# Kernel optimization log

Measured on AMD Instinct MI355X. Metric: run time of the kernel, lower is better.

## Reference

```python
import jax, jax.numpy as jnp
import numpy as np
import math

DIM = 192
D_CONV = 3
EXPAND = 2
D_INNER = EXPAND * DIM          # 384
D_STATE = 1                     # hard-coded in MambaLayer: StructureAwareSSM(..., d_state=1, ...)
DT_RANK = math.ceil(DIM / 16)   # 12
B_, H_, W_ = 16, 96, 96
EPS = 1e-5


def setup_inputs() -> dict:
    key = jax.random.key(0)
    ks = jax.random.split(key, 12)
    s = 0.02
    return {
        "x": jax.random.normal(ks[0], (B_, H_, W_, DIM), jnp.float32),
        "ln_w": jnp.ones((DIM,), jnp.float32),
        "ln_b": jnp.zeros((DIM,), jnp.float32),
        "W_in": jax.random.normal(ks[1], (DIM, 2 * D_INNER), jnp.float32) * s,
        "conv_w": jax.random.normal(ks[2], (D_INNER, 1, D_CONV), jnp.float32) * s,
        "conv_b": jnp.zeros((D_INNER,), jnp.float32),
        "W_xproj": jax.random.normal(ks[3], (D_INNER, DT_RANK + 2 * D_STATE), jnp.float32) * s,
        "W_dt": jax.random.normal(ks[4], (DT_RANK, D_INNER), jnp.float32) * s,
        "b_dt": jax.random.normal(ks[5], (D_INNER,), jnp.float32) * s,
        "A_log": jnp.log(jax.random.uniform(ks[6], (D_INNER, D_STATE), jnp.float32, 0.5, 1.5)),
        "D": jnp.ones((D_INNER,), jnp.float32),
        "W_out": jax.random.normal(ks[7], (D_INNER, DIM), jnp.float32) * s,
    }


def _layernorm(x, w, b):
    mu = x.mean(-1, keepdims=True)
    var = jnp.mean(jnp.square(x - mu), axis=-1, keepdims=True)
    return (x - mu) * jax.lax.rsqrt(var + EPS) * w + b


def _mamba(xs, W_in, conv_w, conv_b, W_xproj, W_dt, b_dt, A_log, D, W_out):
    # xs: (B, L, C)
    b, L, c = xs.shape
    xz = xs @ W_in                                  # (B,L,2*di)
    xb, z = jnp.split(xz, 2, axis=-1)
    # causal depthwise conv over sequence dim
    xc = jax.lax.conv_general_dilated(
        xb.transpose(0, 2, 1),                      # (B,di,L)
        conv_w,                                     # (di,1,k)
        window_strides=(1,),
        padding=[(D_CONV - 1, 0)],
        dimension_numbers=("NCH", "OIH", "NCH"),
        feature_group_count=D_INNER,
    ) + conv_b[None, :, None]
    u = jax.nn.silu(xc).transpose(0, 2, 1)          # (B,L,di)
    proj = u @ W_xproj                              # (B,L,dt_rank+2*ds)
    dt_r = proj[..., :DT_RANK]
    B_ssm = proj[..., DT_RANK:DT_RANK + D_STATE]    # (B,L,ds)
    C_ssm = proj[..., DT_RANK + D_STATE:]           # (B,L,ds)
    dt = jax.nn.softplus(dt_r @ W_dt + b_dt)        # (B,L,di)
    A = -jnp.exp(A_log)                             # (di,ds)
    dA = jnp.exp(dt[..., None] * A)                             # (B,L,di,ds)
    dBu = dt[..., None] * B_ssm[:, :, None, :] * u[..., None]   # (B,L,di,ds)

    def step(h, inp):
        dA_t, dBu_t = inp
        h = dA_t * h + dBu_t
        return h, h

    h0 = jnp.zeros((b, D_INNER, D_STATE), xs.dtype)
    _, hs = jax.lax.scan(step, h0, (dA.transpose(1, 0, 2, 3), dBu.transpose(1, 0, 2, 3)))
    # hs: (L,B,di,ds); contract over state with C
    y = jnp.einsum("lbis,bls->bli", hs, C_ssm)      # (B,L,di)
    y = y + u * D
    y = y * jax.nn.silu(z)
    return y @ W_out                                # (B,L,C)


def reference(x, ln_w, ln_b, W_in, conv_w, conv_b, W_xproj, W_dt, b_dt, A_log, D, W_out):
    b, h, w, c = x.shape
    xn = _layernorm(x, ln_w, ln_b)
    xs = xn.reshape(b, h * w, c)
    y = _mamba(xs, W_in, conv_w, conv_b, W_xproj, W_dt, b_dt, A_log, D, W_out)
    return y.reshape(b, h, w, c) + x
```

## Files before the change

kernel.cpp:

```cpp
#include <hip/hip_runtime.h>
#include <math.h>

#define DIMC 192
#define DIN 384
#define XZC 768
#define NPROJ 14
#define PSTR 16
#define LSEQ 9216
#define NBATCH 16
#define NTOK (NBATCH*LSEQ)
#define CHUNK 128
#define NCH (LSEQ/CHUNK)

typedef unsigned short u16;
typedef unsigned int u32;
typedef __attribute__((ext_vector_type(8))) short bf16x8;
typedef __attribute__((ext_vector_type(4))) float f32x4;

__device__ __forceinline__ float bf2f(u16 a){
  union { u32 u; float f; } v; v.u = ((u32)a)<<16; return v.f;
}
__device__ __forceinline__ u16 f2bf(float f){
  union { u32 u; float f; } v; v.f = f;
  u32 r = v.u + 0x7FFFu + ((v.u>>16)&1u);
  return (u16)(r>>16);
}
__device__ __forceinline__ float frcp(float x){ return __builtin_amdgcn_rcpf(x); }
__device__ __forceinline__ float softplus_f(float x){
  return fmaxf(x, 0.f) + __logf(1.f + __expf(-fabsf(x)));
}
__device__ __forceinline__ float silu_f(float a){
  return a * frcp(1.f + __expf(-a));
}

__global__ void k_convert(const float* __restrict__ Win, const float* __restrict__ Wout,
                          const float* __restrict__ Wx, const float* __restrict__ cw,
                          u16* __restrict__ Bp1, u16* __restrict__ Bp2,
                          u16* __restrict__ Wxp, float* __restrict__ cwT){
  int i = blockIdx.x*256 + threadIdx.x;
  if (i < XZC*DIMC){
    int j = i&7, lane = (i>>3)&63, rest = i>>9;
    int ks = rest%6, nt = rest/6;
    int k = ks*32 + (lane>>4)*8 + j, n = nt*16 + (lane&15);
    Bp1[i] = f2bf(Win[(size_t)k*XZC + n]);
  }
  if (i < DIN*DIMC){
    int j = i&7, lane = (i>>3)&63, rest = i>>9;
    int ks = rest%12, nt = rest/12;
    int k = ks*32 + (lane>>4)*8 + j, n = nt*16 + (lane&15);
    Bp2[i] = f2bf(Wout[(size_t)k*DIMC + n]);
  }
  if (i < 12*4*16*8){
    int j = i&7, n = (i>>3)&15, quad = (i>>7)&3, kstep = i>>9;
    int k = kstep*32 + quad*8 + j;
    Wxp[i] = (n < NPROJ) ? f2bf(Wx[k*NPROJ + n]) : (u16)0;
  }
  if (i < 3*DIN){
    int tap = i / DIN, ch = i - tap*DIN;
    cwT[i] = cw[ch*3 + tap];
  }
}

__global__ __launch_bounds__(256) void k_lngemm1(const float* __restrict__ x,
        const float* __restrict__ lnw, const float* __restrict__ lnb,
        const u16* __restrict__ Bp1, u16* __restrict__ xB, u16* __restrict__ zB)
{
  int tid = threadIdx.x, wv = tid>>6, lane = tid&63;
  int lr = lane&15, lq = lane>>4;
  int tokw = blockIdx.x*128 + wv*32;
  bf16x8 af[2][6];
  #pragma unroll
  for (int s=0;s<2;++s){
    int token = tokw + s*16 + lr;
    const float* xp = x + (size_t)token*DIMC + lq*8;
    float v[48];
    #pragma unroll
    for (int ks=0;ks<6;++ks){
      float4 a = *(const float4*)(xp + ks*32);
      float4 b = *(const float4*)(xp + ks*32 + 4);
      v[ks*8+0]=a.x; v[ks*8+1]=a.y; v[ks*8+2]=a.z; v[ks*8+3]=a.w;
      v[ks*8+4]=b.x; v[ks*8+5]=b.y; v[ks*8+6]=b.z; v[ks*8+7]=b.w;
    }
    float sm = 0.f;
    #pragma unroll
    for (int j=0;j<48;++j) sm += v[j];
    sm += __shfl_xor(sm, 16); sm += __shfl_xor(sm, 32);
    float mu = sm * (1.0f/DIMC);
    float q = 0.f;
    #pragma unroll
    for (int j=0;j<48;++j){ float d = v[j]-mu; q += d*d; }
    q += __shfl_xor(q, 16); q += __shfl_xor(q, 32);
    float rstd = rsqrtf(q*(1.0f/DIMC) + 1e-5f);
    #pragma unroll
    for (int ks=0;ks<6;++ks){
      const float* wp = lnw + lq*8 + ks*32;
      const float* bp = lnb + lq*8 + ks*32;
      float4 w0 = *(const float4*)(wp),   w1 = *(const float4*)(wp+4);
      float4 b0 = *(const float4*)(bp),   b1 = *(const float4*)(bp+4);
      float wj[8] = {w0.x,w0.y,w0.z,w0.w,w1.x,w1.y,w1.z,w1.w};
      float bj[8] = {b0.x,b0.y,b0.z,b0.w,b1.x,b1.y,b1.z,b1.w};
      #pragma unroll
      for (int j=0;j<8;++j)
        af[s][ks][j] = (short)f2bf((v[ks*8+j]-mu)*rstd*wj[j] + bj[j]);
    }
  }
  #pragma unroll 2
  for (int nt=0; nt<48; ++nt){
    f32x4 acc0 = (f32x4){0.f,0.f,0.f,0.f};
    f32x4 acc1 = (f32x4){0.f,0.f,0.f,0.f};
    #pragma unroll
    for (int ks=0;ks<6;++ks){
      bf16x8 bf_ = *(const bf16x8*)(Bp1 + (size_t)((nt*6+ks)<<9) + (size_t)lane*8);
      acc0 = __builtin_amdgcn_mfma_f32_16x16x32_bf16(af[0][ks], bf_, acc0, 0,0,0);
      acc1 = __builtin_amdgcn_mfma_f32_16x16x32_bf16(af[1][ks], bf_, acc1, 0,0,0);
    }
    int col = nt*16 + lr;
    u16* base = (col < DIN) ? xB : zB;
    int cc = (col < DIN) ? col : col - DIN;
    #pragma unroll
    for (int r=0;r<4;++r){
      int row0 = tokw + lq*4 + r;
      base[(size_t)row0*DIN + cc]      = f2bf(acc0[r]);
      base[(size_t)(row0+16)*DIN + cc] = f2bf(acc1[r]);
    }
  }
}

__global__ __launch_bounds__(256) void k_conv(const u16* __restrict__ xB,
        const float* __restrict__ cwT, const float* __restrict__ cb,
        const u16* __restrict__ Wxp, float* __restrict__ proj){
  int tid = threadIdx.x, wv = tid>>6, lane = tid&63;
  int lr = lane&15, lq = lane>>4;
  int tok0 = blockIdx.x*64 + wv*16;
  int token = tok0 + lr;
  int l = token % LSEQ;
  float m1 = (l>=1)?1.f:0.f, m2 = (l>=2)?1.f:0.f;
  int tm1 = (l>=1)? token-1 : token;
  int tm2 = (l>=2)? token-2 : token;
  bf16x8 bfrag[12];
  #pragma unroll
  for (int ks=0;ks<12;++ks)
    bfrag[ks] = *(const bf16x8*)(Wxp + (size_t)ks*512 + (size_t)lane*8);
  f32x4 acc = (f32x4){0.f,0.f,0.f,0.f};
  #pragma unroll
  for (int ks=0;ks<12;++ks){
    int ch0 = ks*32 + lq*8;
    bf16x8 x0 = *(const bf16x8*)(xB + (size_t)token*DIN + ch0);
    bf16x8 x1 = *(const bf16x8*)(xB + (size_t)tm1*DIN + ch0);
    bf16x8 x2 = *(const bf16x8*)(xB + (size_t)tm2*DIN + ch0);
    const float* w2 = cwT + 2*DIN + ch0;
    const float* w1 = cwT + 1*DIN + ch0;
    const float* w0 = cwT + 0*DIN + ch0;
    const float* cbp = cb + ch0;
    bf16x8 af;
    #pragma unroll
    for (int j=0;j<8;++j){
      float a = cbp[j] + w2[j]*bf2f((u16)x0[j])
                       + (w1[j]*m1)*bf2f((u16)x1[j])
                       + (w0[j]*m2)*bf2f((u16)x2[j]);
      af[j] = (short)f2bf(silu_f(a));
    }
    acc = __builtin_amdgcn_mfma_f32_16x16x32_bf16(af, bfrag[ks], acc, 0,0,0);
  }
  #pragma unroll
  for (int r=0;r<4;++r){
    int row = lq*4 + r;
    proj[(size_t)(tok0+row)*PSTR + lr] = acc[r];
  }
}

__global__ __launch_bounds__(384) void k_scan1(const float* __restrict__ proj, const u16* __restrict__ xB,
    const float* __restrict__ cw, const float* __restrict__ cb,
    const float* __restrict__ Wdt, const float* __restrict__ bdt, const float* __restrict__ Alog,
    float* __restrict__ Pg, float* __restrict__ Hg){
  __shared__ __align__(16) float ps[CHUNK*PSTR];
  int b = blockIdx.y, ch = blockIdx.x, d = threadIdx.x;
  int tok0 = b*LSEQ + ch*CHUNK;
  {
    const float4* src = (const float4*)(proj + (size_t)tok0*PSTR);
    float4* dst = (float4*)ps;
    for (int i = d; i < CHUNK*PSTR/4; i += 384) dst[i] = src[i];
  }
  __syncthreads();
  float wdt[12];
  #pragma unroll
  for (int r=0;r<12;++r) wdt[r] = Wdt[r*DIN+d];
  float bd = bdt[d];
  float Av = -__expf(Alog[d]);
  float c0=cw[d*3], c1=cw[d*3+1], c2=cw[d*3+2], cbv=cb[d];
  float xm1=0.f, xm2=0.f;
  if (ch > 0){
    xm1 = bf2f(xB[(size_t)(tok0-1)*DIN + d]);
    xm2 = bf2f(xB[(size_t)(tok0-2)*DIN + d]);
  }
  float h = 0.f, P = 1.f;
  #pragma unroll 4
  for (int il=0; il<CHUNK; ++il){
    float xc = bf2f(xB[(size_t)(tok0+il)*DIN + d]);
    const float4* pq = (const float4*)(ps + il*PSTR);
    float4 q0=pq[0], q1=pq[1], q2=pq[2], q3=pq[3];
    float a = cbv + c2*xc + c1*xm1 + c0*xm2;
    float uu = silu_f(a);
    float xv = bd + q0.x*wdt[0]+q0.y*wdt[1]+q0.z*wdt[2]+q0.w*wdt[3]
                  + q1.x*wdt[4]+q1.y*wdt[5]+q1.z*wdt[6]+q1.w*wdt[7]
                  + q2.x*wdt[8]+q2.y*wdt[9]+q2.z*wdt[10]+q2.w*wdt[11];
    float dt = softplus_f(xv);
    float dA = __expf(dt*Av);
    h = dA*h + dt*q3.x*uu;
    P *= dA;
    xm2 = xm1; xm1 = xc;
  }
  int o = (b*NCH + ch)*DIN + d;
  Pg[o] = P; Hg[o] = h;
}

__global__ void k_scan2(const float* __restrict__ Pg, const float* __restrict__ Hg,
                        float* __restrict__ hin){
  int idx = blockIdx.x*256 + threadIdx.x;
  int b = idx/DIN, d = idx - b*DIN;
  float run = 0.f;
  #pragma unroll 4
  for (int ch=0; ch<NCH; ++ch){
    int o = (b*NCH+ch)*DIN + d;
    hin[o] = run;
    run = Pg[o]*run + Hg[o];
  }
}

__global__ __launch_bounds__(384) void k_scan3(const float* __restrict__ proj, const u16* __restrict__ xB,
    const float* __restrict__ cw, const float* __restrict__ cb,
    const float* __restrict__ Wdt, const float* __restrict__ bdt,
    const float* __restrict__ Alog, const float* __restrict__ Dp,
    const float* __restrict__ hin, u16* __restrict__ zB){
  __shared__ __align__(16) float ps[CHUNK*PSTR];
  int b = blockIdx.y, ch = blockIdx.x, d = threadIdx.x;
  int tok0 = b*LSEQ + ch*CHUNK;
  {
    const float4* src = (const float4*)(proj + (size_t)tok0*PSTR);
    float4* dst = (float4*)ps;
    for (int i = d; i < CHUNK*PSTR/4; i += 384) dst[i] = src[i];
  }
  __syncthreads();
  float wdt[12];
  #pragma unroll
  for (int r=0;r<12;++r) wdt[r] = Wdt[r*DIN+d];
  float bd = bdt[d];
  float Av = -__expf(Alog[d]);
  float Dv = Dp[d];
  float c0=cw[d*3], c1=cw[d*3+1], c2=cw[d*3+2], cbv=cb[d];
  float xm1=0.f, xm2=0.f;
  if (ch > 0){
    xm1 = bf2f(xB[(size_t)(tok0-1)*DIN + d]);
    xm2 = bf2f(xB[(size_t)(tok0-2)*DIN + d]);
  }
  float h = hin[(b*NCH+ch)*DIN + d];
  #pragma unroll 4
  for (int il=0; il<CHUNK; ++il){
    float xc = bf2f(xB[(size_t)(tok0+il)*DIN + d]);
    const float4* pq = (const float4*)(ps + il*PSTR);
    float4 q0=pq[0], q1=pq[1], q2=pq[2], q3=pq[3];
    float a = cbv + c2*xc + c1*xm1 + c0*xm2;
    float uu = silu_f(a);
    float xv = bd + q0.x*wdt[0]+q0.y*wdt[1]+q0.z*wdt[2]+q0.w*wdt[3]
                  + q1.x*wdt[4]+q1.y*wdt[5]+q1.z*wdt[6]+q1.w*wdt[7]
                  + q2.x*wdt[8]+q2.y*wdt[9]+q2.z*wdt[10]+q2.w*wdt[11];
    float dt = softplus_f(xv);
    float dA = __expf(dt*Av);
    h = dA*h + dt*q3.x*uu;
    size_t zo = (size_t)(tok0+il)*DIN + d;
    float zz = bf2f(zB[zo]);
    zB[zo] = f2bf((h*q3.y + uu*Dv)*silu_f(zz));
    xm2 = xm1; xm1 = xc;
  }
}

__global__ __launch_bounds__(256) void k_gemm2(const u16* __restrict__ A, const u16* __restrict__ Bp2,
        const float* __restrict__ R, float* __restrict__ C)
{
  int tid = threadIdx.x, wv = tid>>6, lane = tid&63;
  int lr = lane&15, lq = lane>>4;
  int tokw = blockIdx.x*128 + wv*32;
  int t0 = tokw + lr, t1 = tokw + 16 + lr;
  bf16x8 af0[12], af1[12];
  #pragma unroll
  for (int ks=0;ks<12;++ks){
    af0[ks] = *(const bf16x8*)(A + (size_t)t0*DIN + ks*32 + lq*8);
    af1[ks] = *(const bf16x8*)(A + (size_t)t1*DIN + ks*32 + lq*8);
  }
  #pragma unroll 2
  for (int nt=0; nt<12; ++nt){
    f32x4 acc0 = (f32x4){0.f,0.f,0.f,0.f};
    f32x4 acc1 = (f32x4){0.f,0.f,0.f,0.f};
    #pragma unroll
    for (int ks=0;ks<12;++ks){
      bf16x8 bf_ = *(const bf16x8*)(Bp2 + (size_t)((nt*12+ks)<<9) + (size_t)lane*8);
      acc0 = __builtin_amdgcn_mfma_f32_16x16x32_bf16(af0[ks], bf_, acc0, 0,0,0);
      acc1 = __builtin_amdgcn_mfma_f32_16x16x32_bf16(af1[ks], bf_, acc1, 0,0,0);
    }
    int col = nt*16 + lr;
    #pragma unroll
    for (int r=0;r<4;++r){
      int row = tokw + lq*4 + r;
      size_t o0 = (size_t)row*DIMC + col;
      size_t o1 = (size_t)(row+16)*DIMC + col;
      C[o0] = acc0[r] + R[o0];
      C[o1] = acc1[r] + R[o1];
    }
  }
}

extern "C" void kernel_launch(void* const* d_in, const int* in_sizes, int n_in,
                              void* d_out, int out_size, void* d_ws, size_t ws_size,
                              hipStream_t stream) {
  const float* x     = (const float*)d_in[0];
  const float* lnw   = (const float*)d_in[1];
  const float* lnb   = (const float*)d_in[2];
  const float* Win   = (const float*)d_in[3];
  const float* convw = (const float*)d_in[4];
  const float* convb = (const float*)d_in[5];
  const float* Wx    = (const float*)d_in[6];
  const float* Wdt   = (const float*)d_in[7];
  const float* bdt   = (const float*)d_in[8];
  const float* Alog  = (const float*)d_in[9];
  const float* Dp    = (const float*)d_in[10];
  const float* Wout  = (const float*)d_in[11];
  float* out = (float*)d_out;

  char* ws = (char*)d_ws;
  size_t off = 0;
  auto alloc = [&](size_t bytes){ size_t r = off; off += (bytes + 255) & ~(size_t)255; return r; };
  u16*   xB    = (u16*)  (ws + alloc((size_t)NTOK*DIN*2));
  u16*   zB    = (u16*)  (ws + alloc((size_t)NTOK*DIN*2));
  float* proj  = (float*)(ws + alloc((size_t)NTOK*PSTR*4));
  u16*   Bp1   = (u16*)  (ws + alloc((size_t)XZC*DIMC*2));
  u16*   Bp2   = (u16*)  (ws + alloc((size_t)DIN*DIMC*2));
  u16*   Wxp   = (u16*)  (ws + alloc((size_t)12*4*16*8*2));
  float* cwT   = (float*)(ws + alloc((size_t)3*DIN*4));
  float* Pg    = (float*)(ws + alloc((size_t)NBATCH*NCH*DIN*4));
  float* Hg    = (float*)(ws + alloc((size_t)NBATCH*NCH*DIN*4));
  float* hin   = (float*)(ws + alloc((size_t)NBATCH*NCH*DIN*4));

  k_convert<<<576, 256, 0, stream>>>(Win, Wout, Wx, convw, Bp1, Bp2, Wxp, cwT);
  k_lngemm1<<<NTOK/128, 256, 0, stream>>>(x, lnw, lnb, Bp1, xB, zB);
  k_conv<<<NTOK/64, 256, 0, stream>>>(xB, cwT, convb, Wxp, proj);
  {
    dim3 g(NCH, NBATCH);
    k_scan1<<<g, 384, 0, stream>>>(proj, xB, convw, convb, Wdt, bdt, Alog, Pg, Hg);
  }
  k_scan2<<<24, 256, 0, stream>>>(Pg, Hg, hin);
  {
    dim3 g(NCH, NBATCH);
    k_scan3<<<g, 384, 0, stream>>>(proj, xB, convw, convb, Wdt, bdt, Alog, Dp, hin, zB);
  }
  k_gemm2<<<NTOK/128, 256, 0, stream>>>(zB, Bp2, x, out);
}
```

Before: 737.4 us.

## Stage GEMM weights in LDS and materialize conv output for scans

```diff
diff --git a/kernel.cpp b/kernel.cpp
--- a/kernel.cpp
+++ b/kernel.cpp
@@ -17,6 +17,9 @@
 typedef __attribute__((ext_vector_type(8))) short bf16x8;
 typedef __attribute__((ext_vector_type(4))) float f32x4;
 
+#define AS1 __attribute__((address_space(1)))
+#define AS3 __attribute__((address_space(3)))
+
 __device__ __forceinline__ float bf2f(u16 a){
   union { u32 u; float f; } v; v.u = ((u32)a)<<16; return v.f;
 }
@@ -61,13 +64,14 @@
   }
 }
 
-__global__ __launch_bounds__(256) void k_lngemm1(const float* __restrict__ x,
+__global__ __launch_bounds__(512) void k_lngemm1(const float* __restrict__ x,
         const float* __restrict__ lnw, const float* __restrict__ lnb,
         const u16* __restrict__ Bp1, u16* __restrict__ xB, u16* __restrict__ zB)
 {
+  __shared__ __align__(16) char smem[49152];
   int tid = threadIdx.x, wv = tid>>6, lane = tid&63;
   int lr = lane&15, lq = lane>>4;
-  int tokw = blockIdx.x*128 + wv*32;
+  int tokw = blockIdx.x*256 + wv*32;
   bf16x8 af[2][6];
   #pragma unroll
   for (int s=0;s<2;++s){
@@ -104,31 +108,45 @@
         af[s][ks][j] = (short)f2bf((v[ks*8+j]-mu)*rstd*wj[j] + bj[j]);
     }
   }
-  #pragma unroll 2
-  for (int nt=0; nt<48; ++nt){
-    f32x4 acc0 = (f32x4){0.f,0.f,0.f,0.f};
-    f32x4 acc1 = (f32x4){0.f,0.f,0.f,0.f};
-    #pragma unroll
-    for (int ks=0;ks<6;++ks){
-      bf16x8 bf_ = *(const bf16x8*)(Bp1 + (size_t)((nt*6+ks)<<9) + (size_t)lane*8);
-      acc0 = __builtin_amdgcn_mfma_f32_16x16x32_bf16(af[0][ks], bf_, acc0, 0,0,0);
-      acc1 = __builtin_amdgcn_mfma_f32_16x16x32_bf16(af[1][ks], bf_, acc1, 0,0,0);
-    }
-    int col = nt*16 + lr;
-    u16* base = (col < DIN) ? xB : zB;
-    int cc = (col < DIN) ? col : col - DIN;
-    #pragma unroll
-    for (int r=0;r<4;++r){
-      int row0 = tokw + lq*4 + r;
-      base[(size_t)row0*DIN + cc]      = f2bf(acc0[r]);
-      base[(size_t)(row0+16)*DIN + cc] = f2bf(acc1[r]);
-    }
+  for (int c=0;c<6;++c){
+    {
+      const u16* gsrc = Bp1 + (size_t)c*24576 + wv*3072 + lane*8;
+      char* lbase = smem + wv*6144;
+      #pragma unroll
+      for (int r=0;r<6;++r)
+        __builtin_amdgcn_global_load_lds((const AS1 void*)(gsrc + r*512),
+                                         (AS3 void*)(lbase + r*1024), 16, 0, 0);
+    }
+    asm volatile("s_waitcnt vmcnt(0)" ::: "memory");
+    __syncthreads();
+    #pragma unroll
+    for (int ntl=0; ntl<8; ++ntl){
+      int nt = c*8 + ntl;
+      f32x4 acc0 = (f32x4){0.f,0.f,0.f,0.f};
+      f32x4 acc1 = (f32x4){0.f,0.f,0.f,0.f};
+      #pragma unroll
+      for (int ks=0;ks<6;++ks){
+        bf16x8 bf_ = *(const bf16x8*)(smem + ((ntl*6+ks)<<10) + lane*16);
+        acc0 = __builtin_amdgcn_mfma_f32_16x16x32_bf16(af[0][ks], bf_, acc0, 0,0,0);
+        acc1 = __builtin_amdgcn_mfma_f32_16x16x32_bf16(af[1][ks], bf_, acc1, 0,0,0);
+      }
+      int col = nt*16 + lr;
+      u16* base = (col < DIN) ? xB : zB;
+      int cc = (col < DIN) ? col : col - DIN;
+      #pragma unroll
+      for (int r=0;r<4;++r){
+        int row0 = tokw + lq*4 + r;
+        base[(size_t)row0*DIN + cc]      = f2bf(acc0[r]);
+        base[(size_t)(row0+16)*DIN + cc] = f2bf(acc1[r]);
+      }
+    }
+    __syncthreads();
   }
 }
 
 __global__ __launch_bounds__(256) void k_conv(const u16* __restrict__ xB,
         const float* __restrict__ cwT, const float* __restrict__ cb,
-        const u16* __restrict__ Wxp, float* __restrict__ proj){
+        const u16* __restrict__ Wxp, float* __restrict__ proj, u16* __restrict__ uB){
   int tid = threadIdx.x, wv = tid>>6, lane = tid&63;
   int lr = lane&15, lq = lane>>4;
   int tok0 = blockIdx.x*64 + wv*16;
@@ -160,6 +178,7 @@
                        + (w0[j]*m2)*bf2f((u16)x2[j]);
       af[j] = (short)f2bf(silu_f(a));
     }
+    *(bf16x8*)(uB + (size_t)token*DIN + ch0) = af;
     acc = __builtin_amdgcn_mfma_f32_16x16x32_bf16(af, bfrag[ks], acc, 0,0,0);
   }
   #pragma unroll
@@ -169,8 +188,7 @@
   }
 }
 
-__global__ __launch_bounds__(384) void k_scan1(const float* __restrict__ proj, const u16* __restrict__ xB,
-    const float* __restrict__ cw, const float* __restrict__ cb,
+__global__ __launch_bounds__(384) void k_scan1(const float* __restrict__ proj, const u16* __restrict__ uB,
     const float* __restrict__ Wdt, const float* __restrict__ bdt, const float* __restrict__ Alog,
     float* __restrict__ Pg, float* __restrict__ Hg){
   __shared__ __align__(16) float ps[CHUNK*PSTR];
@@ -187,20 +205,12 @@
   for (int r=0;r<12;++r) wdt[r] = Wdt[r*DIN+d];
   float bd = bdt[d];
   float Av = -__expf(Alog[d]);
-  float c0=cw[d*3], c1=cw[d*3+1], c2=cw[d*3+2], cbv=cb[d];
-  float xm1=0.f, xm2=0.f;
-  if (ch > 0){
-    xm1 = bf2f(xB[(size_t)(tok0-1)*DIN + d]);
-    xm2 = bf2f(xB[(size_t)(tok0-2)*DIN + d]);
-  }
   float h = 0.f, P = 1.f;
   #pragma unroll 4
   for (int il=0; il<CHUNK; ++il){
-    float xc = bf2f(xB[(size_t)(tok0+il)*DIN + d]);
+    float uu = bf2f(uB[(size_t)(tok0+il)*DIN + d]);
     const float4* pq = (const float4*)(ps + il*PSTR);
     float4 q0=pq[0], q1=pq[1], q2=pq[2], q3=pq[3];
-    float a = cbv + c2*xc + c1*xm1 + c0*xm2;
-    float uu = silu_f(a);
     float xv = bd + q0.x*wdt[0]+q0.y*wdt[1]+q0.z*wdt[2]+q0.w*wdt[3]
                   + q1.x*wdt[4]+q1.y*wdt[5]+q1.z*wdt[6]+q1.w*wdt[7]
                   + q2.x*wdt[8]+q2.y*wdt[9]+q2.z*wdt[10]+q2.w*wdt[11];
@@ -208,7 +218,6 @@
     float dA = __expf(dt*Av);
     h = dA*h + dt*q3.x*uu;
     P *= dA;
-    xm2 = xm1; xm1 = xc;
   }
   int o = (b*NCH + ch)*DIN + d;
   Pg[o] = P; Hg[o] = h;
@@ -227,8 +236,7 @@
   }
 }
 
-__global__ __launch_bounds__(384) void k_scan3(const float* __restrict__ proj, const u16* __restrict__ xB,
-    const float* __restrict__ cw, const float* __restrict__ cb,
+__global__ __launch_bounds__(384) void k_scan3(const float* __restrict__ proj, const u16* __restrict__ uB,
     const float* __restrict__ Wdt, const float* __restrict__ bdt,
     const float* __restrict__ Alog, const float* __restrict__ Dp,
     const float* __restrict__ hin, u16* __restrict__ zB){
@@ -247,20 +255,12 @@
   float bd = bdt[d];
   float Av = -__expf(Alog[d]);
   float Dv = Dp[d];
-  float c0=cw[d*3], c1=cw[d*3+1], c2=cw[d*3+2], cbv=cb[d];
-  float xm1=0.f, xm2=0.f;
-  if (ch > 0){
-    xm1 = bf2f(xB[(size_t)(tok0-1)*DIN + d]);
-    xm2 = bf2f(xB[(size_t)(tok0-2)*DIN + d]);
-  }
   float h = hin[(b*NCH+ch)*DIN + d];
   #pragma unroll 4
   for (int il=0; il<CHUNK; ++il){
-    float xc = bf2f(xB[(size_t)(tok0+il)*DIN + d]);
+    float uu = bf2f(uB[(size_t)(tok0+il)*DIN + d]);
     const float4* pq = (const float4*)(ps + il*PSTR);
     float4 q0=pq[0], q1=pq[1], q2=pq[2], q3=pq[3];
-    float a = cbv + c2*xc + c1*xm1 + c0*xm2;
-    float uu = silu_f(a);
     float xv = bd + q0.x*wdt[0]+q0.y*wdt[1]+q0.z*wdt[2]+q0.w*wdt[3]
                   + q1.x*wdt[4]+q1.y*wdt[5]+q1.z*wdt[6]+q1.w*wdt[7]
                   + q2.x*wdt[8]+q2.y*wdt[9]+q2.z*wdt[10]+q2.w*wdt[11];
@@ -270,42 +270,50 @@
     size_t zo = (size_t)(tok0+il)*DIN + d;
     float zz = bf2f(zB[zo]);
     zB[zo] = f2bf((h*q3.y + uu*Dv)*silu_f(zz));
-    xm2 = xm1; xm1 = xc;
-  }
-}
-
-__global__ __launch_bounds__(256) void k_gemm2(const u16* __restrict__ A, const u16* __restrict__ Bp2,
+  }
+}
+
+__global__ __launch_bounds__(512) void k_gemm2(const u16* __restrict__ A, const u16* __restrict__ Bp2,
         const float* __restrict__ R, float* __restrict__ C)
 {
+  __shared__ __align__(16) char smem[49152];
   int tid = threadIdx.x, wv = tid>>6, lane = tid&63;
   int lr = lane&15, lq = lane>>4;
-  int tokw = blockIdx.x*128 + wv*32;
-  int t0 = tokw + lr, t1 = tokw + 16 + lr;
-  bf16x8 af0[12], af1[12];
-  #pragma unroll
-  for (int ks=0;ks<12;++ks){
-    af0[ks] = *(const bf16x8*)(A + (size_t)t0*DIN + ks*32 + lq*8);
-    af1[ks] = *(const bf16x8*)(A + (size_t)t1*DIN + ks*32 + lq*8);
-  }
-  #pragma unroll 2
-  for (int nt=0; nt<12; ++nt){
-    f32x4 acc0 = (f32x4){0.f,0.f,0.f,0.f};
-    f32x4 acc1 = (f32x4){0.f,0.f,0.f,0.f};
-    #pragma unroll
-    for (int ks=0;ks<12;++ks){
-      bf16x8 bf_ = *(const bf16x8*)(Bp2 + (size_t)((nt*12+ks)<<9) + (size_t)lane*8);
-      acc0 = __builtin_amdgcn_mfma_f32_16x16x32_bf16(af0[ks], bf_, acc0, 0,0,0);
-      acc1 = __builtin_amdgcn_mfma_f32_16x16x32_bf16(af1[ks], bf_, acc1, 0,0,0);
-    }
-    int col = nt*16 + lr;
-    #pragma unroll
-    for (int r=0;r<4;++r){
-      int row = tokw + lq*4 + r;
-      size_t o0 = (size_t)row*DIMC + col;
-      size_t o1 = (size_t)(row+16)*DIMC + col;
-      C[o0] = acc0[r] + R[o0];
-      C[o1] = acc1[r] + R[o1];
-    }
+  int tokw = blockIdx.x*128 + wv*16;
+  int token = tokw + lr;
+  bf16x8 af[12];
+  #pragma unroll
+  for (int ks=0;ks<12;++ks)
+    af[ks] = *(const bf16x8*)(A + (size_t)token*DIN + ks*32 + lq*8);
+  for (int c=0;c<3;++c){
+    {
+      const u16* gsrc = Bp2 + (size_t)c*24576 + wv*3072 + lane*8;
+      char* lbase = smem + wv*6144;
+      #pragma unroll
+      for (int r=0;r<6;++r)
+        __builtin_amdgcn_global_load_lds((const AS1 void*)(gsrc + r*512),
+                                         (AS3 void*)(lbase + r*1024), 16, 0, 0);
+    }
+    asm volatile("s_waitcnt vmcnt(0)" ::: "memory");
+    __syncthreads();
+    #pragma unroll
+    for (int ntl=0; ntl<4; ++ntl){
+      int nt = c*4 + ntl;
+      f32x4 acc = (f32x4){0.f,0.f,0.f,0.f};
+      #pragma unroll
+      for (int ks=0;ks<12;++ks){
+        bf16x8 bf_ = *(const bf16x8*)(smem + ((ntl*12+ks)<<10) + lane*16);
+        acc = __builtin_amdgcn_mfma_f32_16x16x32_bf16(af[ks], bf_, acc, 0,0,0);
+      }
+      int col = nt*16 + lr;
+      #pragma unroll
+      for (int r=0;r<4;++r){
+        int row = tokw + lq*4 + r;
+        size_t o = (size_t)row*DIMC + col;
+        C[o] = acc[r] + R[o];
+      }
+    }
+    __syncthreads();
   }
 }
 
@@ -331,6 +339,7 @@
   auto alloc = [&](size_t bytes){ size_t r = off; off += (bytes + 255) & ~(size_t)255; return r; };
   u16*   xB    = (u16*)  (ws + alloc((size_t)NTOK*DIN*2));
   u16*   zB    = (u16*)  (ws + alloc((size_t)NTOK*DIN*2));
+  u16*   uB    = (u16*)  (ws + alloc((size_t)NTOK*DIN*2));
   float* proj  = (float*)(ws + alloc((size_t)NTOK*PSTR*4));
   u16*   Bp1   = (u16*)  (ws + alloc((size_t)XZC*DIMC*2));
   u16*   Bp2   = (u16*)  (ws + alloc((size_t)DIN*DIMC*2));
@@ -341,16 +350,16 @@
   float* hin   = (float*)(ws + alloc((size_t)NBATCH*NCH*DIN*4));
 
   k_convert<<<576, 256, 0, stream>>>(Win, Wout, Wx, convw, Bp1, Bp2, Wxp, cwT);
-  k_lngemm1<<<NTOK/128, 256, 0, stream>>>(x, lnw, lnb, Bp1, xB, zB);
-  k_conv<<<NTOK/64, 256, 0, stream>>>(xB, cwT, convb, Wxp, proj);
+  k_lngemm1<<<NTOK/256, 512, 0, stream>>>(x, lnw, lnb, Bp1, xB, zB);
+  k_conv<<<NTOK/64, 256, 0, stream>>>(xB, cwT, convb, Wxp, proj, uB);
   {
     dim3 g(NCH, NBATCH);
-    k_scan1<<<g, 384, 0, stream>>>(proj, xB, convw, convb, Wdt, bdt, Alog, Pg, Hg);
+    k_scan1<<<g, 384, 0, stream>>>(proj, uB, Wdt, bdt, Alog, Pg, Hg);
   }
   k_scan2<<<24, 256, 0, stream>>>(Pg, Hg, hin);
   {
     dim3 g(NCH, NBATCH);
-    k_scan3<<<g, 384, 0, stream>>>(proj, xB, convw, convb, Wdt, bdt, Alog, Dp, hin, zB);
-  }
-  k_gemm2<<<NTOK/128, 256, 0, stream>>>(zB, Bp2, x, out);
-}
+    k_scan3<<<g, 384, 0, stream>>>(proj, uB, Wdt, bdt, Alog, Dp, hin, zB);
+  }
+  k_gemm2<<<NTOK/128, 512, 0, stream>>>(zB, Bp2, x, out);
+}
```

Result: faster. 670.9 us (-9.0%).
